# Performance work log

Hardware: AMD Instinct MI355X
Metric: run time of the kernel (lower is better)

The kernel has to match this reference:

```python
import jax, jax.numpy as jnp
import numpy as np

NEG_INF = -1e9  # matches tf mask value -1000000000.0
LEAKY_ALPHA = 0.2  # tf.nn.leaky_relu default


def setup_inputs() -> dict:
    key = jax.random.key(0)
    k1, k2, k3, k4 = jax.random.split(key, 4)
    B, N, F, U = 8, 2048, 128, 128
    X = jax.random.normal(k1, (B, N, F), dtype=jnp.float32)
    A = jax.random.randint(k2, (B, N, N), 0, 2, dtype=jnp.int32)
    W = jax.random.normal(k3, (F, U), dtype=jnp.float32) * 0.1
    a = jax.random.normal(k4, (2 * U, 1), dtype=jnp.float32) * 0.1
    return {"X": X, "A": A, "W": W, "a": a}


def reference(X, A, W, a):
    # H = X @ W : [B, N, U]
    H = jnp.einsum('bnf,fu->bnu', X, W)
    U = H.shape[-1]
    # Additive decomposition of the tile+concat: [H_i || H_j] @ a = H_i@a_src + H_j@a_dst
    a_src = a[:U, 0]   # [U]
    a_dst = a[U:, 0]   # [U]
    s = H @ a_src      # [B, N]
    t = H @ a_dst      # [B, N]
    e = s[:, :, None] + t[:, None, :]            # [B, N, N] pairwise logits
    e = jax.nn.leaky_relu(e, negative_slope=LEAKY_ALPHA)
    mask = jnp.where(A > 0, 0.0, NEG_INF).astype(e.dtype)
    attention = jax.nn.softmax(e + mask, axis=-1)  # [B, N, N]
    H_out = jnp.einsum('bij,bju->biu', attention, H)
    return jax.nn.relu(H_out)
```

## Files before the change

kernel.cpp:

```cpp
#include <hip/hip_runtime.h>
#include <hip/hip_bf16.h>


#define NEG_INF -1.0e9f

typedef __bf16 bf16x8 __attribute__((ext_vector_type(8)));
typedef unsigned short ushort8 __attribute__((ext_vector_type(8)));
typedef float f32x4 __attribute__((ext_vector_type(4)));

__device__ __forceinline__ unsigned short f2b(float x) {
    unsigned u = __builtin_bit_cast(unsigned, x);
    u += 0x7fffu + ((u >> 16) & 1u);
    return (unsigned short)(u >> 16);
}

__device__ __forceinline__ void gload_lds16(const void* g, void* l) {
    __builtin_amdgcn_global_load_lds(
        (const __attribute__((address_space(1))) void*)g,
        (__attribute__((address_space(3))) void*)l, 16, 0, 0);
}

__global__ __launch_bounds__(256) void k_wt(const float* __restrict__ W,
                                            unsigned short* __restrict__ WT) {
    int tid = blockIdx.x * 256 + threadIdx.x;
    int u = tid >> 7, f = tid & 127;
    WT[tid] = f2b(W[f * 128 + u]);
}

__global__ __launch_bounds__(256) void k_h_pack(const float* __restrict__ X,
                                                const unsigned short* __restrict__ WT,
                                                const float* __restrict__ a,
                                                const int* __restrict__ A,
                                                unsigned short* __restrict__ HT,
                                                float* __restrict__ sbuf,
                                                float* __restrict__ tbuf,
                                                unsigned int* __restrict__ Abits) {
    const int tid  = threadIdx.x;
    const int w    = tid >> 6;
    const int lane = tid & 63;

    if (blockIdx.x < 1024) {
        const int wid = blockIdx.x * 4 + w;
#pragma unroll 2
        for (int rr = 0; rr < 4; ++rr) {
            const int row = wid * 4 + rr;
            const int* Ap = A + (size_t)row * 2048 + lane * 32;
            unsigned int word = 0;
#pragma unroll
            for (int kk = 0; kk < 8; ++kk) {
                int4 v = *(const int4*)(Ap + kk * 4);
                word |= (v.x > 0 ? 1u : 0u) << (kk * 4 + 0);
                word |= (v.y > 0 ? 1u : 0u) << (kk * 4 + 1);
                word |= (v.z > 0 ? 1u : 0u) << (kk * 4 + 2);
                word |= (v.w > 0 ? 1u : 0u) << (kk * 4 + 3);
            }
            Abits[(size_t)row * 64 + lane] = word;
        }
        return;
    }

    const int r    = lane & 15;
    const int cg   = lane >> 4;
    const int row0 = (blockIdx.x - 1024) * 64 + w * 16;
    const int b    = row0 >> 11;
    const int n0   = row0 & 2047;
    const int arow = row0 + r;

    f32x4 acc[8] = {};

#pragma unroll
    for (int k0 = 0; k0 < 128; k0 += 32) {
        const float* xp = X + (size_t)arow * 128 + k0 + cg * 8;
        ushort8 xa;
#pragma unroll
        for (int j = 0; j < 8; j++) xa[j] = f2b(xp[j]);
        bf16x8 av = __builtin_bit_cast(bf16x8, xa);
#pragma unroll
        for (int ut = 0; ut < 8; ut++) {
            ushort8 wb = *(const ushort8*)(WT + (size_t)(ut * 16 + r) * 128 + k0 + cg * 8);
            acc[ut] = __builtin_amdgcn_mfma_f32_16x16x32_bf16(
                av, __builtin_bit_cast(bf16x8, wb), acc[ut], 0, 0, 0);
        }
    }

    float sp[4] = {0.f, 0.f, 0.f, 0.f};
    float tp[4] = {0.f, 0.f, 0.f, 0.f};
#pragma unroll
    for (int ut = 0; ut < 8; ut++) {
        int u = ut * 16 + r;
        float as = a[u];
        float ad = a[128 + u];
#pragma unroll
        for (int reg = 0; reg < 4; reg++) {
            float h = acc[ut][reg];
            int nrow = n0 + cg * 4 + reg;
            HT[((size_t)b * 128 + u) * 2048 + nrow] = f2b(h);
            sp[reg] += h * as;
            tp[reg] += h * ad;
        }
    }
#pragma unroll
    for (int msk = 1; msk < 16; msk <<= 1) {
#pragma unroll
        for (int reg = 0; reg < 4; reg++) {
            sp[reg] += __shfl_xor(sp[reg], msk);
            tp[reg] += __shfl_xor(tp[reg], msk);
        }
    }
    if (r == 0) {
#pragma unroll
        for (int reg = 0; reg < 4; reg++) {
            int row = row0 + cg * 4 + reg;
            sbuf[row] = sp[reg];
            tbuf[row] = tp[reg];
        }
    }
}

__global__ __launch_bounds__(512, 4) void k_attn(const unsigned int* __restrict__ Abits,
                                                 const unsigned short* __restrict__ HT,
                                                 const float* __restrict__ sbuf,
                                                 const float* __restrict__ tbuf,
                                                 float* __restrict__ out) {
    __shared__ char smem[65536];
    __shared__ float tS[2048];
    __shared__ float dSm[4][2][16];

    const int tid  = threadIdx.x;
    const int w    = tid >> 6;
    const int lane = tid & 63;
    const int r    = lane & 15;
    const int cg   = lane >> 4;
    const int g    = w & 1;
    const int jq   = w >> 1;
    const int bid  = blockIdx.x;
    const int b    = bid & 7;
    const int it   = bid >> 3;
    const int i0   = it * 32;
    const int rot  = it & 15;

    const int irow = i0 + g * 16 + r;
    const float s_r = sbuf[b * 2048 + irow];
    const unsigned int* Mrow = Abits + ((size_t)(b * 2048 + irow)) * 64 + jq * 16;
    const unsigned short* Hb = HT + ((size_t)b * 128) * 2048 + jq * 512;

    const int srow = (lane >> 2);
    const int csrc = (lane & 3) ^ ((lane >> 2) & 3) ^ ((lane >> 4) & 3);
    char* const qbase = smem + jq * 16384;
    const unsigned short* src0 = Hb + (size_t)(g * 64 + srow) * 2048 + csrc * 8;
    const int rsl = ((r & 3) ^ ((r >> 2) & 3));

    f32x4 acc[8] = {};
    float den = 0.f;

    *(float4*)(tS + tid * 4) = *(const float4*)(tbuf + b * 2048 + tid * 4);

    unsigned int mw = Mrow[rot];
    {
        const int j0 = rot * 32;
#pragma unroll
        for (int i = 0; i < 4; i++)
            gload_lds16(src0 + (size_t)i * 16 * 2048 + j0,
                        qbase + (g * 4 + i) * 1024);
    }
    __syncthreads();

    for (int k = 0; k < 16; ++k) {
        const int p = k & 1;
        unsigned int mwn = 0;
        if (k < 15) {
            const int kn = (k + 1 + rot) & 15;
            char* dst = qbase + (p ^ 1) * 8192;
#pragma unroll
            for (int i = 0; i < 4; i++)
                gload_lds16(src0 + (size_t)i * 16 * 2048 + kn * 32,
                            dst + (g * 4 + i) * 1024);
            mwn = Mrow[kn];
        }

        const float* tq = tS + jq * 512 + ((k + rot) & 15) * 32 + cg * 8;
        float4 t0 = *(const float4*)(tq);
        float4 t1 = *(const float4*)(tq + 4);
        float tv[8] = {t0.x, t0.y, t0.z, t0.w, t1.x, t1.y, t1.z, t1.w};
        const unsigned int sh = mw >> (cg * 8);
        bf16x8 pa;
#pragma unroll
        for (int jj = 0; jj < 8; jj++) {
            float x = s_r + tv[jj];
            float e = fmaxf(x, 0.2f * x);
            float pp = __expf(e - 16.0f);
            pp = ((sh >> jj) & 1u) ? pp : 0.f;
            den += pp;
            pa[jj] = (__bf16)pp;
        }

        const char* buf = qbase + p * 8192;
#pragma unroll
        for (int ut = 0; ut < 8; ut++) {
            ushort8 hb = *(const ushort8*)(buf + (ut * 16 + r) * 64 +
                                           ((cg ^ rsl) * 16));
            acc[ut] = __builtin_amdgcn_mfma_f32_16x16x32_bf16(
                pa, __builtin_bit_cast(bf16x8, hb), acc[ut], 0, 0, 0);
        }

        mw = mwn;
        __syncthreads();
    }

    den += __shfl_xor(den, 16);
    den += __shfl_xor(den, 32);

    float* accS = (float*)smem;
    if (cg == 0) dSm[jq][g][r] = den;
    if (jq != 0) {
        const int rowIdx = ((jq - 1) * 2 + g) * 16 + cg * 4;
#pragma unroll
        for (int ut = 0; ut < 8; ut++)
#pragma unroll
            for (int reg = 0; reg < 4; reg++)
                accS[(rowIdx + reg) * 132 + ut * 16 + r] = acc[ut][reg];
    }
    __syncthreads();
    if (jq == 0) {
        float dinv[4];
#pragma unroll
        for (int reg = 0; reg < 4; reg++) {
            const int row = cg * 4 + reg;
            dinv[reg] = 1.0f / (dSm[0][g][row] + dSm[1][g][row] +
                                dSm[2][g][row] + dSm[3][g][row]);
        }
#pragma unroll
        for (int ut = 0; ut < 8; ut++) {
#pragma unroll
            for (int reg = 0; reg < 4; reg++) {
                const int lrow = cg * 4 + reg;
                float num = acc[ut][reg]
                          + accS[((0 * 2 + g) * 16 + lrow) * 132 + ut * 16 + r]
                          + accS[((1 * 2 + g) * 16 + lrow) * 132 + ut * 16 + r]
                          + accS[((2 * 2 + g) * 16 + lrow) * 132 + ut * 16 + r];
                float o = fmaxf(num * dinv[reg], 0.f);
                out[((size_t)(b * 2048 + i0 + g * 16 + lrow)) * 128 +
                    ut * 16 + r] = o;
            }
        }
    }
}

extern "C" void kernel_launch(void* const* d_in, const int* in_sizes, int n_in,
                              void* d_out, int out_size, void* d_ws, size_t ws_size,
                              hipStream_t stream) {
    const float* X = (const float*)d_in[0];
    const int*   A = (const int*)d_in[1];
    const float* W = (const float*)d_in[2];
    const float* a = (const float*)d_in[3];
    float* out = (float*)d_out;

    char* ws = (char*)d_ws;
    unsigned short* WT  = (unsigned short*)(ws);
    float*          sb  = (float*)(ws + 32768);
    float*          tb  = (float*)(ws + 98304);
    unsigned short* HT  = (unsigned short*)(ws + 163840);
    unsigned int*   Ab  = (unsigned int*)(ws + 163840 + 4194304);

    k_wt<<<dim3(64), dim3(256), 0, stream>>>(W, WT);
    k_h_pack<<<dim3(1280), dim3(256), 0, stream>>>(X, WT, a, A, HT, sb, tb, Ab);
    k_attn<<<dim3(512), dim3(512), 0, stream>>>(Ab, HT, sb, tb, out);
}
```

Measured before the change: 70.75 us.

## Fuse adjacency bit-packing into attention kernel and drop global bitmask buffer

Moves conversion of the int32 adjacency rows into bitmasks from the H-projection kernel into the attention kernel. Each attention block now packs its own 32 rows into shared memory and pulls per-thread mask words into registers before the main loop. This removes the global write and re-read of the packed bitmask, and shrinks the projection launch to only the H/s/t work. In exchange, the attention kernel's prologue now streams the full A slice before compute starts, and the main loop is fully unrolled, which could raise register pressure.

```diff
diff --git a/kernel.cpp b/kernel.cpp
--- a/kernel.cpp
+++ b/kernel.cpp
@@ -27,41 +27,18 @@
     WT[tid] = f2b(W[f * 128 + u]);
 }
 
-__global__ __launch_bounds__(256) void k_h_pack(const float* __restrict__ X,
-                                                const unsigned short* __restrict__ WT,
-                                                const float* __restrict__ a,
-                                                const int* __restrict__ A,
-                                                unsigned short* __restrict__ HT,
-                                                float* __restrict__ sbuf,
-                                                float* __restrict__ tbuf,
-                                                unsigned int* __restrict__ Abits) {
+__global__ __launch_bounds__(256) void k_h(const float* __restrict__ X,
+                                           const unsigned short* __restrict__ WT,
+                                           const float* __restrict__ a,
+                                           unsigned short* __restrict__ HT,
+                                           float* __restrict__ sbuf,
+                                           float* __restrict__ tbuf) {
     const int tid  = threadIdx.x;
     const int w    = tid >> 6;
     const int lane = tid & 63;
-
-    if (blockIdx.x < 1024) {
-        const int wid = blockIdx.x * 4 + w;
-#pragma unroll 2
-        for (int rr = 0; rr < 4; ++rr) {
-            const int row = wid * 4 + rr;
-            const int* Ap = A + (size_t)row * 2048 + lane * 32;
-            unsigned int word = 0;
-#pragma unroll
-            for (int kk = 0; kk < 8; ++kk) {
-                int4 v = *(const int4*)(Ap + kk * 4);
-                word |= (v.x > 0 ? 1u : 0u) << (kk * 4 + 0);
-                word |= (v.y > 0 ? 1u : 0u) << (kk * 4 + 1);
-                word |= (v.z > 0 ? 1u : 0u) << (kk * 4 + 2);
-                word |= (v.w > 0 ? 1u : 0u) << (kk * 4 + 3);
-            }
-            Abits[(size_t)row * 64 + lane] = word;
-        }
-        return;
-    }
-
     const int r    = lane & 15;
     const int cg   = lane >> 4;
-    const int row0 = (blockIdx.x - 1024) * 64 + w * 16;
+    const int row0 = blockIdx.x * 64 + w * 16;
     const int b    = row0 >> 11;
     const int n0   = row0 & 2047;
     const int arow = row0 + r;
@@ -117,7 +94,7 @@
     }
 }
 
-__global__ __launch_bounds__(512, 4) void k_attn(const unsigned int* __restrict__ Abits,
+__global__ __launch_bounds__(512, 4) void k_attn(const int* __restrict__ A,
                                                  const unsigned short* __restrict__ HT,
                                                  const float* __restrict__ sbuf,
                                                  const float* __restrict__ tbuf,
@@ -141,8 +118,34 @@
 
     const int irow = i0 + g * 16 + r;
     const float s_r = sbuf[b * 2048 + irow];
-    const unsigned int* Mrow = Abits + ((size_t)(b * 2048 + irow)) * 64 + jq * 16;
     const unsigned short* Hb = HT + ((size_t)b * 128) * 2048 + jq * 512;
+
+    unsigned int* bitsS = (unsigned int*)smem;
+    {
+        const int* Abase = A + ((size_t)(b * 2048 + i0 + w * 4)) * 2048;
+#pragma unroll
+        for (int rr = 0; rr < 4; ++rr) {
+            const int* Ap = Abase + rr * 2048 + lane * 32;
+            unsigned int word = 0;
+#pragma unroll
+            for (int kk = 0; kk < 8; ++kk) {
+                int4 v = *(const int4*)(Ap + kk * 4);
+                word |= (v.x > 0 ? 1u : 0u) << (kk * 4 + 0);
+                word |= (v.y > 0 ? 1u : 0u) << (kk * 4 + 1);
+                word |= (v.z > 0 ? 1u : 0u) << (kk * 4 + 2);
+                word |= (v.w > 0 ? 1u : 0u) << (kk * 4 + 3);
+            }
+            bitsS[(w * 4 + rr) * 65 + lane] = word;
+        }
+    }
+    *(float4*)(tS + tid * 4) = *(const float4*)(tbuf + b * 2048 + tid * 4);
+    __syncthreads();
+
+    unsigned int wordsR[16];
+#pragma unroll
+    for (int k = 0; k < 16; ++k)
+        wordsR[k] = bitsS[(g * 16 + r) * 65 + jq * 16 + ((k + rot) & 15)];
+    __syncthreads();
 
     const int srow = (lane >> 2);
     const int csrc = (lane & 3) ^ ((lane >> 2) & 3) ^ ((lane >> 4) & 3);
@@ -153,9 +156,6 @@
     f32x4 acc[8] = {};
     float den = 0.f;
 
-    *(float4*)(tS + tid * 4) = *(const float4*)(tbuf + b * 2048 + tid * 4);
-
-    unsigned int mw = Mrow[rot];
     {
         const int j0 = rot * 32;
 #pragma unroll
@@ -165,9 +165,9 @@
     }
     __syncthreads();
 
+#pragma unroll
     for (int k = 0; k < 16; ++k) {
         const int p = k & 1;
-        unsigned int mwn = 0;
         if (k < 15) {
             const int kn = (k + 1 + rot) & 15;
             char* dst = qbase + (p ^ 1) * 8192;
@@ -175,14 +175,13 @@
             for (int i = 0; i < 4; i++)
                 gload_lds16(src0 + (size_t)i * 16 * 2048 + kn * 32,
                             dst + (g * 4 + i) * 1024);
-            mwn = Mrow[kn];
         }
 
         const float* tq = tS + jq * 512 + ((k + rot) & 15) * 32 + cg * 8;
         float4 t0 = *(const float4*)(tq);
         float4 t1 = *(const float4*)(tq + 4);
         float tv[8] = {t0.x, t0.y, t0.z, t0.w, t1.x, t1.y, t1.z, t1.w};
-        const unsigned int sh = mw >> (cg * 8);
+        const unsigned int sh = wordsR[k] >> (cg * 8);
         bf16x8 pa;
 #pragma unroll
         for (int jj = 0; jj < 8; jj++) {
@@ -203,7 +202,6 @@
                 pa, __builtin_bit_cast(bf16x8, hb), acc[ut], 0, 0, 0);
         }
 
-        mw = mwn;
         __syncthreads();
     }
 
@@ -260,9 +258,8 @@
     float*          sb  = (float*)(ws + 32768);
     float*          tb  = (float*)(ws + 98304);
     unsigned short* HT  = (unsigned short*)(ws + 163840);
-    unsigned int*   Ab  = (unsigned int*)(ws + 163840 + 4194304);
 
     k_wt<<<dim3(64), dim3(256), 0, stream>>>(W, WT);
-    k_h_pack<<<dim3(1280), dim3(256), 0, stream>>>(X, WT, a, A, HT, sb, tb, Ab);
-    k_attn<<<dim3(512), dim3(512), 0, stream>>>(Ab, HT, sb, tb, out);
-}
+    k_h<<<dim3(256), dim3(256), 0, stream>>>(X, WT, a, HT, sb, tb);
+    k_attn<<<dim3(512), dim3(512), 0, stream>>>(A, HT, sb, tb, out);
+}
```

New measurement: 65.38 us. -7.6%, faster.
